# Performance work log

Measured on AMD Instinct MI355X. Metric: run time of the kernel, lower is better.

Reference implementation:

```python
import jax, jax.numpy as jnp
import numpy as np

N_HEADS = 16


def setup_inputs() -> dict:
    key = jax.random.key(0)
    ks = jax.random.split(key, 4)
    B, S, E = 4, 2048, 1024
    x = jax.random.normal(ks[0], (B, S, E), dtype=jnp.float32)
    w_attn = jax.random.normal(ks[1], (E, 3 * E), dtype=jnp.float32) * 0.02
    b_attn = jnp.zeros((3 * E,), dtype=jnp.float32)
    w_proj = jax.random.normal(ks[2], (E, E), dtype=jnp.float32) * 0.02
    b_proj = jnp.zeros((E,), dtype=jnp.float32)
    return {"x": x, "w_attn": w_attn, "b_attn": b_attn, "w_proj": w_proj, "b_proj": b_proj}


def reference(x, w_attn, b_attn, w_proj, b_proj):
    B, S, E = x.shape
    H = N_HEADS
    D = E // H
    # fused QKV projection (Conv1D: x @ W + b)
    qkv = x @ w_attn + b_attn                     # [B, S, 3E]
    q, k, v = jnp.split(qkv, 3, axis=-1)          # each [B, S, E]
    q = q.reshape(B, S, H, D).transpose(0, 2, 1, 3)  # [B, H, S, D]
    k = k.reshape(B, S, H, D).transpose(0, 2, 1, 3)
    v = v.reshape(B, S, H, D).transpose(0, 2, 1, 3)
    # scaled QK^T
    scores = jnp.einsum('bhqd,bhkd->bhqk', q, k) / jnp.sqrt(jnp.asarray(D, dtype=x.dtype))
    # causal mask via where with dtype-min fill (matches torch.where(c_m, w, finfo.min))
    causal = jnp.tril(jnp.ones((S, S), dtype=bool))  # [S, S]
    scores = jnp.where(causal[None, None, :, :], scores, jnp.finfo(scores.dtype).min)
    attn = jax.nn.softmax(scores, axis=-1)        # [B, H, S, S]
    o = jnp.einsum('bhqk,bhkd->bhqd', attn, v)    # [B, H, S, D]
    o = o.transpose(0, 2, 1, 3).reshape(B, S, E)  # merge heads
    return o @ w_proj + b_proj                    # output projection
```

## Files before the change

kernel.cpp:

```cpp
#include <hip/hip_runtime.h>
#include <stdint.h>


typedef __bf16 bf16;
typedef __bf16 bf16x4 __attribute__((ext_vector_type(4)));
typedef __bf16 bf16x8 __attribute__((ext_vector_type(8)));
typedef float  f32x4  __attribute__((ext_vector_type(4)));

#define DEV __device__ __forceinline__

DEV void async_copy16(bf16* lds, const bf16* g) {
  __builtin_amdgcn_global_load_lds(
      (__attribute__((address_space(1))) void*)(uintptr_t)g,
      (__attribute__((address_space(3))) void*)(uint32_t)(uintptr_t)lds,
      16, 0, 0);
}

__global__ __launch_bounds__(256) void cast_x_kernel(const float* __restrict__ in,
                                                     bf16* __restrict__ out, int n4) {
  int i = blockIdx.x * blockDim.x + threadIdx.x;
  int stride = gridDim.x * blockDim.x;
  for (; i < n4; i += stride) {
    float4 v = ((const float4*)in)[i];
    bf16x4 o = { (bf16)v.x, (bf16)v.y, (bf16)v.z, (bf16)v.w };
    *(bf16x4*)(out + (size_t)i * 4) = o;
  }
}

__global__ __launch_bounds__(256) void transpose_cast_kernel(const float* __restrict__ W,
                                                             bf16* __restrict__ Wt,
                                                             int Kd, int Nd) {
  __shared__ alignas(16) bf16 T[64 * 80];
  const int t = threadIdx.x;
  const int n0 = blockIdx.x * 64;
  const int k0 = blockIdx.y * 64;
#pragma unroll
  for (int i = 0; i < 4; ++i) {
    int idx = t + i * 256;
    int r  = idx >> 4;
    int c4 = (idx & 15) * 4;
    float4 v = *(const float4*)(W + (size_t)(k0 + r) * Nd + n0 + c4);
    bf16x4 o = { (bf16)v.x, (bf16)v.y, (bf16)v.z, (bf16)v.w };
    *(bf16x4*)(&T[r * 80 + c4]) = o;
  }
  __syncthreads();
#pragma unroll
  for (int i = 0; i < 2; ++i) {
    int idx = t + i * 256;
    int n = idx >> 3;
    int c = idx & 7;
    bf16x8 o;
#pragma unroll
    for (int j = 0; j < 8; ++j) o[j] = T[(c * 8 + j) * 80 + n];
    *(bf16x8*)(Wt + (size_t)(n0 + n) * Kd + k0 + c * 8) = o;
  }
}

template <typename OutT, bool FUSE_VT>
__global__ __launch_bounds__(512, 4) void gemm256_kernel(const bf16* __restrict__ A,
                                                         const bf16* __restrict__ Bt,
                                                         const float* __restrict__ bias,
                                                         OutT* __restrict__ C,
                                                         bf16* __restrict__ vtout,
                                                         int M, int N, int K,
                                                         float qscale, int qcols,
                                                         int nbx) {
  __shared__ alignas(16) bf16 As[3][256 * 32];
  __shared__ alignas(16) bf16 Bs[3][128 * 32];

  const int tid  = threadIdx.x;
  const int lane = tid & 63;
  const int w    = tid >> 6;
  const int wm = w >> 1, wn = w & 1;
  const int l15 = lane & 15, l16 = lane >> 4;

  const int nwg = (int)gridDim.x;
  const int cpx = nwg >> 3;
  const int swz = ((int)blockIdx.x & 7) * cpx + ((int)blockIdx.x >> 3);
  const int m0 = (swz / nbx) * 256;
  const int n0 = (swz % nbx) * 128;

  const int c0  = w * 64 + lane;
  const int rA0 = c0 >> 2, sA0 = c0 & 3;
  const int rA1 = rA0 + 128;
  const bf16* srcA0 = A  + (size_t)(m0 + rA0) * K + 8 * (sA0 ^ ((rA0 >> 1) & 3));
  const bf16* srcA1 = A  + (size_t)(m0 + rA1) * K + 8 * (sA0 ^ ((rA1 >> 1) & 3));
  const bf16* srcB  = Bt + (size_t)(n0 + rA0) * K + 8 * (sA0 ^ ((rA0 >> 1) & 3));

#define STAGE_TILE(buf, kt)                                       \
  {                                                               \
    const int k0_ = (kt) * 32;                                    \
    async_copy16(&As[buf][(w * 64) * 8],         srcA0 + k0_);    \
    async_copy16(&As[buf][(512 + w * 64) * 8],   srcA1 + k0_);    \
    async_copy16(&Bs[buf][(w * 64) * 8],         srcB  + k0_);    \
  }

  f32x4 acc[4][4];
  f32x4 zf = {0.f, 0.f, 0.f, 0.f};
#pragma unroll
  for (int i = 0; i < 4; ++i)
#pragma unroll
    for (int j = 0; j < 4; ++j) acc[i][j] = zf;

  const int KT = K >> 5;
  STAGE_TILE(0, 0)
  STAGE_TILE(1, 1)

  const int soff = 8 * (l16 ^ ((l15 >> 1) & 3));

  int bufc = 0;
  int bufs = 2;
  for (int kt = 0; kt < KT; ++kt) {
    if (kt < KT - 1) { asm volatile("s_waitcnt vmcnt(3)" ::: "memory"); }
    else             { asm volatile("s_waitcnt vmcnt(0)" ::: "memory"); }
    __builtin_amdgcn_s_barrier();
    asm volatile("" ::: "memory");
    if (kt + 2 < KT) STAGE_TILE(bufs, kt + 2)

    bf16x8 bfr[4], afr[4];
#pragma unroll
    for (int n = 0; n < 4; ++n) {
      int rb = wn * 64 + n * 16 + l15;
      bfr[n] = *(const bf16x8*)(&Bs[bufc][rb * 32 + soff]);
    }
#pragma unroll
    for (int m = 0; m < 4; ++m) {
      int ra = wm * 64 + m * 16 + l15;
      afr[m] = *(const bf16x8*)(&As[bufc][ra * 32 + soff]);
    }
    __builtin_amdgcn_s_setprio(1);
#pragma unroll
    for (int m = 0; m < 4; ++m)
#pragma unroll
      for (int n = 0; n < 4; ++n)
        acc[m][n] = __builtin_amdgcn_mfma_f32_16x16x32_bf16(afr[m], bfr[n], acc[m][n], 0, 0, 0);
    __builtin_amdgcn_s_setprio(0);
    asm volatile("" ::: "memory");
    bufc = (bufc == 2) ? 0 : bufc + 1;
    bufs = (bufs == 2) ? 0 : bufs + 1;
  }

#pragma unroll
  for (int n = 0; n < 4; ++n) {
    int col = n0 + wn * 64 + n * 16 + l15;
    float bb = bias[col];
    if (FUSE_VT && col >= 2048) {
      int hh = (col - 2048) >> 6, d = (col - 2048) & 63;
#pragma unroll
      for (int m = 0; m < 4; ++m) {
#pragma unroll
        for (int reg = 0; reg < 4; ++reg) {
          int row = m0 + wm * 64 + m * 16 + l16 * 4 + reg;
          int s = row & 2047;
          int key = s & 63;
          int pos = (key & 32) | (((key >> 2) & 3) << 3) | (((key >> 4) & 1) << 2) | (key & 3);
          size_t vtaddr = ((size_t)((row >> 11) * 16 + hh) * 64 + d) * 2048 + (s & ~63) + pos;
          vtout[vtaddr] = (bf16)(acc[m][n][reg] + bb);
        }
      }
    } else {
      float sc2 = (col < qcols) ? qscale : 1.0f;
#pragma unroll
      for (int m = 0; m < 4; ++m) {
#pragma unroll
        for (int reg = 0; reg < 4; ++reg) {
          int row = m0 + wm * 64 + m * 16 + l16 * 4 + reg;
          C[(size_t)row * N + col] = (OutT)((acc[m][n][reg] + bb) * sc2);
        }
      }
    }
  }
#undef STAGE_TILE
}

__global__ __launch_bounds__(256, 4) void flash_kernel(const bf16* __restrict__ qkv,
                                                       const bf16* __restrict__ vt,
                                                       bf16* __restrict__ obuf) {
  constexpr int S = 2048, E3 = 3072;
  __shared__ alignas(16) bf16 Ks[2][64 * 64];
  __shared__ alignas(16) bf16 Vs[2][64 * 64];

  const int tid  = threadIdx.x;
  const int lane = tid & 63;
  const int w    = tid >> 6;
  const int t  = 15 - (int)blockIdx.x;
  const int bh = blockIdx.y;
  const int b = bh >> 4, h = bh & 15;
  const int l15 = lane & 15, l16 = lane >> 4;

  const int sr  = lane >> 3;
  const int scc = lane & 7;
  const int r0 = w * 16 + sr;
  const int r1 = w * 16 + 8 + sr;
  const bf16* kst0 = qkv + (size_t)(b * S + r0) * E3 + 1024 + h * 64 + 8 * (scc ^ sr);
  const bf16* kst1 = qkv + (size_t)(b * S + r1) * E3 + 1024 + h * 64 + 8 * (scc ^ sr);
  const bf16* vst0 = vt + (size_t)(bh * 64 + r0) * S + 8 * (scc ^ sr);
  const bf16* vst1 = vt + (size_t)(bh * 64 + r1) * S + 8 * (scc ^ sr);

  const int xsw = l15 & 7;
  const uint32_t rdA = (uint32_t)(l15 * 128 + 16 * (l16 ^ xsw));
  const uint32_t rdB = (uint32_t)(l15 * 128 + 16 * ((4 + l16) ^ xsw));

#define KV_STAGE(buf, kv0_)                                          \
  {                                                                  \
    async_copy16(Ks[buf] + (w * 2) * 512,     kst0 + (size_t)(kv0_) * E3); \
    async_copy16(Ks[buf] + (w * 2 + 1) * 512, kst1 + (size_t)(kv0_) * E3); \
    async_copy16(Vs[buf] + (w * 2) * 512,     vst0 + (kv0_));        \
    async_copy16(Vs[buf] + (w * 2 + 1) * 512, vst1 + (kv0_));        \
  }

  const int q0 = t * 128;
  const int wq0 = q0 + w * 32;
  const int nsteps = 2 * t + 2;

  KV_STAGE(0, 0)

  bf16x8 qf[2][2];
  {
    const bf16* qbase = qkv + (size_t)(b * S + wq0) * E3 + h * 64;
#pragma unroll
    for (int s = 0; s < 2; ++s)
#pragma unroll
      for (int dk = 0; dk < 2; ++dk)
        qf[s][dk] = *(const bf16x8*)(qbase + (size_t)(s * 16 + l15) * E3 + (dk * 4 + l16) * 8);
  }

  float lstate[2] = {0.f, 0.f};
  f32x4 oacc[2][4];
  f32x4 zf = {0.f, 0.f, 0.f, 0.f};
#pragma unroll
  for (int s = 0; s < 2; ++s)
#pragma unroll
    for (int i = 0; i < 4; ++i) oacc[s][i] = zf;

  __syncthreads();

#define FLASH_STEP(CUR, STEPIDX)                                                  \
    {                                                                             \
      const int kv0 = (STEPIDX) * 64;                                             \
      if ((STEPIDX) + 1 < nsteps) KV_STAGE((CUR) ^ 1, kv0 + 64)                   \
      if (kv0 <= wq0 + 31) {                     \
        f32x4 sv[2][4];                                                           \
        _Pragma("unroll")                                                         \
        for (int kf = 0; kf < 4; ++kf) { sv[0][kf] = zf; sv[1][kf] = zf; }        \
        __builtin_amdgcn_s_setprio(1);                                            \
        _Pragma("unroll")                                                         \
        for (int kf = 0; kf < 4; ++kf) {                                          \
          bf16x8 k0 = *(const bf16x8*)((const char*)Ks[CUR] + rdA + kf * 2048);   \
          sv[0][kf] = __builtin_amdgcn_mfma_f32_16x16x32_bf16(k0, qf[0][0], sv[0][kf], 0, 0, 0); \
          sv[1][kf] = __builtin_amdgcn_mfma_f32_16x16x32_bf16(k0, qf[1][0], sv[1][kf], 0, 0, 0); \
          bf16x8 k1 = *(const bf16x8*)((const char*)Ks[CUR] + rdB + kf * 2048);   \
          sv[0][kf] = __builtin_amdgcn_mfma_f32_16x16x32_bf16(k1, qf[0][1], sv[0][kf], 0, 0, 0); \
          sv[1][kf] = __builtin_amdgcn_mfma_f32_16x16x32_bf16(k1, qf[1][1], sv[1][kf], 0, 0, 0); \
        }                                                                         \
        __builtin_amdgcn_s_setprio(0);                                            \
        bf16x8 pb[2][2];                                                          \
        _Pragma("unroll")                                                         \
        for (int s = 0; s < 2; ++s) {                                             \
          if (kv0 + 63 > wq0 + s * 16) {                \
            const int qrow_ = wq0 + s * 16 + l15;                                 \
            _Pragma("unroll")                                                     \
            for (int kf = 0; kf < 4; ++kf)                                        \
              _Pragma("unroll")                                                   \
              for (int reg = 0; reg < 4; ++reg) {                                 \
                int key = kv0 + kf * 16 + l16 * 4 + reg;                          \
                if (key > qrow_) sv[s][kf][reg] = -1e30f;                         \
              }                                                                   \
          }                                                                       \
          float rsum = 0.f;                                                       \
          _Pragma("unroll")                                                       \
          for (int kf = 0; kf < 4; ++kf)                                          \
            _Pragma("unroll")                                                     \
            for (int reg = 0; reg < 4; ++reg) {                                   \
              float p = __builtin_amdgcn_exp2f(sv[s][kf][reg]);                   \
              sv[s][kf][reg] = p;                                                 \
              rsum += p;                                                          \
            }                                                                     \
          rsum += __shfl_xor(rsum, 16);                                           \
          rsum += __shfl_xor(rsum, 32);                                           \
          lstate[s] += rsum;                                                      \
          _Pragma("unroll")                                                       \
          for (int kc = 0; kc < 2; ++kc) {                                        \
            bf16x8 tq;                                                            \
            tq[0] = (bf16)sv[s][2 * kc][0];  tq[1] = (bf16)sv[s][2 * kc][1];      \
            tq[2] = (bf16)sv[s][2 * kc][2];  tq[3] = (bf16)sv[s][2 * kc][3];      \
            tq[4] = (bf16)sv[s][2 * kc + 1][0]; tq[5] = (bf16)sv[s][2 * kc + 1][1]; \
            tq[6] = (bf16)sv[s][2 * kc + 1][2]; tq[7] = (bf16)sv[s][2 * kc + 1][3]; \
            pb[s][kc] = tq;                                                       \
          }                                                                       \
        }                                                                         \
        __builtin_amdgcn_s_setprio(1);                                            \
        _Pragma("unroll")                                                         \
        for (int nf = 0; nf < 4; ++nf) {                                          \
          bf16x8 vf0 = *(const bf16x8*)((const char*)Vs[CUR] + rdA + nf * 2048);  \
          oacc[0][nf] = __builtin_amdgcn_mfma_f32_16x16x32_bf16(vf0, pb[0][0], oacc[0][nf], 0, 0, 0); \
          oacc[1][nf] = __builtin_amdgcn_mfma_f32_16x16x32_bf16(vf0, pb[1][0], oacc[1][nf], 0, 0, 0); \
          bf16x8 vf1 = *(const bf16x8*)((const char*)Vs[CUR] + rdB + nf * 2048);  \
          oacc[0][nf] = __builtin_amdgcn_mfma_f32_16x16x32_bf16(vf1, pb[0][1], oacc[0][nf], 0, 0, 0); \
          oacc[1][nf] = __builtin_amdgcn_mfma_f32_16x16x32_bf16(vf1, pb[1][1], oacc[1][nf], 0, 0, 0); \
        }                                                                         \
        __builtin_amdgcn_s_setprio(0);                                            \
      }                                                                           \
      __syncthreads();          \
    }

  for (int step = 0; step < nsteps; step += 2) {
    FLASH_STEP(0, step)
    FLASH_STEP(1, step + 1)
  }
#undef FLASH_STEP

#pragma unroll
  for (int s = 0; s < 2; ++s) {
    float inv = 1.0f / lstate[s];
    int qrow = wq0 + s * 16 + l15;
#pragma unroll
    for (int nf = 0; nf < 4; ++nf) {
      bf16x4 o4 = { (bf16)(oacc[s][nf][0] * inv), (bf16)(oacc[s][nf][1] * inv),
                    (bf16)(oacc[s][nf][2] * inv), (bf16)(oacc[s][nf][3] * inv) };
      *(bf16x4*)(obuf + (size_t)(b * S + qrow) * 1024 + h * 64 + nf * 16 + l16 * 4) = o4;
    }
  }
#undef KV_STAGE
}

extern "C" void kernel_launch(void* const* d_in, const int* in_sizes, int n_in,
                              void* d_out, int out_size, void* d_ws, size_t ws_size,
                              hipStream_t stream) {
  (void)in_sizes; (void)n_in; (void)out_size; (void)ws_size;
  const float* x      = (const float*)d_in[0];
  const float* w_attn = (const float*)d_in[1];
  const float* b_attn = (const float*)d_in[2];
  const float* w_proj = (const float*)d_in[3];
  const float* b_proj = (const float*)d_in[4];
  float* out = (float*)d_out;

  char* ws = (char*)d_ws;
  bf16* xb  = (bf16*)(ws + 0);
  bf16* wat = (bf16*)(ws + 16777216);
  bf16* wpt = (bf16*)(ws + 23068672);
  bf16* qkv = (bf16*)(ws + 25165824);
  bf16* vt  = (bf16*)(ws + 75497472);
  bf16* ob  = (bf16*)(ws + 92274688);

  const float QSCALE = 0.18033688011112042f;

  cast_x_kernel<<<2048, 256, 0, stream>>>(x, xb, 8192 * 1024 / 4);
  transpose_cast_kernel<<<dim3(48, 16), 256, 0, stream>>>(w_attn, wat, 1024, 3072);
  transpose_cast_kernel<<<dim3(16, 16), 256, 0, stream>>>(w_proj, wpt, 1024, 1024);
  gemm256_kernel<bf16, true><<<768, 512, 0, stream>>>(xb, wat, b_attn, qkv, vt,
                                                      8192, 3072, 1024, QSCALE, 1024, 24);
  flash_kernel<<<dim3(16, 64), 256, 0, stream>>>(qkv, vt, ob);
  gemm256_kernel<float, false><<<256, 512, 0, stream>>>(ob, wpt, b_proj, out, nullptr,
                                                        8192, 1024, 1024, 1.0f, 0, 8);
}
```

Before: 173.0 us.

## Pair causal query tiles per block and triple-buffer KV with one barrier per step

Each flash block now handles two query tiles (t and 15-t), so every block does the same amount of causal work and the grid is halved. KV staging moves from double to triple buffering with a prefetch distance of two tiles. Explicit vmcnt waits plus a single barrier per step replace the trailing __syncthreads. This targets causal load imbalance and exposed load latency, at the cost of more LDS per block (possibly lower occupancy) and fewer blocks, which leaves less parallelism.

```diff
diff --git a/kernel.cpp b/kernel.cpp
--- a/kernel.cpp
+++ b/kernel.cpp
@@ -177,13 +177,13 @@
                                                        const bf16* __restrict__ vt,
                                                        bf16* __restrict__ obuf) {
   constexpr int S = 2048, E3 = 3072;
-  __shared__ alignas(16) bf16 Ks[2][64 * 64];
-  __shared__ alignas(16) bf16 Vs[2][64 * 64];
+  __shared__ alignas(16) bf16 Ks[3][64 * 64];
+  __shared__ alignas(16) bf16 Vs[3][64 * 64];
 
   const int tid  = threadIdx.x;
   const int lane = tid & 63;
   const int w    = tid >> 6;
-  const int t  = 15 - (int)blockIdx.x;
+  const int bx = blockIdx.x;
   const int bh = blockIdx.y;
   const int b = bh >> 4, h = bh & 15;
   const int l15 = lane & 15, l16 = lane >> 4;
@@ -209,116 +209,129 @@
     async_copy16(Vs[buf] + (w * 2 + 1) * 512, vst1 + (kv0_));        \
   }
 
-  const int q0 = t * 128;
-  const int wq0 = q0 + w * 32;
-  const int nsteps = 2 * t + 2;
-
-  KV_STAGE(0, 0)
-
-  bf16x8 qf[2][2];
-  {
-    const bf16* qbase = qkv + (size_t)(b * S + wq0) * E3 + h * 64;
+  for (int half = 0; half < 2; ++half) {
+    const int t = half ? (15 - bx) : bx;
+    const int q0 = t * 128;
+    const int wq0 = q0 + w * 32;
+    const int nsteps = 2 * t + 2;
+
+    KV_STAGE(0, 0)
+    KV_STAGE(1, 64)
+
+    bf16x8 qf[2][2];
+    {
+      const bf16* qbase = qkv + (size_t)(b * S + wq0) * E3 + h * 64;
+#pragma unroll
+      for (int s = 0; s < 2; ++s)
+#pragma unroll
+        for (int dk = 0; dk < 2; ++dk)
+          qf[s][dk] = *(const bf16x8*)(qbase + (size_t)(s * 16 + l15) * E3 + (dk * 4 + l16) * 8);
+    }
+
+    float lstate[2] = {0.f, 0.f};
+    f32x4 oacc[2][4];
+    f32x4 zf = {0.f, 0.f, 0.f, 0.f};
 #pragma unroll
     for (int s = 0; s < 2; ++s)
 #pragma unroll
-      for (int dk = 0; dk < 2; ++dk)
-        qf[s][dk] = *(const bf16x8*)(qbase + (size_t)(s * 16 + l15) * E3 + (dk * 4 + l16) * 8);
-  }
-
-  float lstate[2] = {0.f, 0.f};
-  f32x4 oacc[2][4];
-  f32x4 zf = {0.f, 0.f, 0.f, 0.f};
-#pragma unroll
-  for (int s = 0; s < 2; ++s)
-#pragma unroll
-    for (int i = 0; i < 4; ++i) oacc[s][i] = zf;
-
-  __syncthreads();
-
-#define FLASH_STEP(CUR, STEPIDX)                                                  \
-    {                                                                             \
-      const int kv0 = (STEPIDX) * 64;                                             \
-      if ((STEPIDX) + 1 < nsteps) KV_STAGE((CUR) ^ 1, kv0 + 64)                   \
-      if (kv0 <= wq0 + 31) {                     \
-        f32x4 sv[2][4];                                                           \
-        _Pragma("unroll")                                                         \
-        for (int kf = 0; kf < 4; ++kf) { sv[0][kf] = zf; sv[1][kf] = zf; }        \
-        __builtin_amdgcn_s_setprio(1);                                            \
-        _Pragma("unroll")                                                         \
-        for (int kf = 0; kf < 4; ++kf) {                                          \
-          bf16x8 k0 = *(const bf16x8*)((const char*)Ks[CUR] + rdA + kf * 2048);   \
-          sv[0][kf] = __builtin_amdgcn_mfma_f32_16x16x32_bf16(k0, qf[0][0], sv[0][kf], 0, 0, 0); \
-          sv[1][kf] = __builtin_amdgcn_mfma_f32_16x16x32_bf16(k0, qf[1][0], sv[1][kf], 0, 0, 0); \
-          bf16x8 k1 = *(const bf16x8*)((const char*)Ks[CUR] + rdB + kf * 2048);   \
-          sv[0][kf] = __builtin_amdgcn_mfma_f32_16x16x32_bf16(k1, qf[0][1], sv[0][kf], 0, 0, 0); \
-          sv[1][kf] = __builtin_amdgcn_mfma_f32_16x16x32_bf16(k1, qf[1][1], sv[1][kf], 0, 0, 0); \
-        }                                                                         \
-        __builtin_amdgcn_s_setprio(0);                                            \
-        bf16x8 pb[2][2];                                                          \
-        _Pragma("unroll")                                                         \
-        for (int s = 0; s < 2; ++s) {                                             \
-          if (kv0 + 63 > wq0 + s * 16) {                \
-            const int qrow_ = wq0 + s * 16 + l15;                                 \
-            _Pragma("unroll")                                                     \
-            for (int kf = 0; kf < 4; ++kf)                                        \
-              _Pragma("unroll")                                                   \
-              for (int reg = 0; reg < 4; ++reg) {                                 \
-                int key = kv0 + kf * 16 + l16 * 4 + reg;                          \
-                if (key > qrow_) sv[s][kf][reg] = -1e30f;                         \
-              }                                                                   \
-          }                                                                       \
-          float rsum = 0.f;                                                       \
-          _Pragma("unroll")                                                       \
-          for (int kf = 0; kf < 4; ++kf)                                          \
-            _Pragma("unroll")                                                     \
-            for (int reg = 0; reg < 4; ++reg) {                                   \
-              float p = __builtin_amdgcn_exp2f(sv[s][kf][reg]);                   \
-              sv[s][kf][reg] = p;                                                 \
-              rsum += p;                                                          \
-            }                                                                     \
-          rsum += __shfl_xor(rsum, 16);                                           \
-          rsum += __shfl_xor(rsum, 32);                                           \
-          lstate[s] += rsum;                                                      \
-          _Pragma("unroll")                                                       \
-          for (int kc = 0; kc < 2; ++kc) {                                        \
-            bf16x8 tq;                                                            \
-            tq[0] = (bf16)sv[s][2 * kc][0];  tq[1] = (bf16)sv[s][2 * kc][1];      \
-            tq[2] = (bf16)sv[s][2 * kc][2];  tq[3] = (bf16)sv[s][2 * kc][3];      \
-            tq[4] = (bf16)sv[s][2 * kc + 1][0]; tq[5] = (bf16)sv[s][2 * kc + 1][1]; \
-            tq[6] = (bf16)sv[s][2 * kc + 1][2]; tq[7] = (bf16)sv[s][2 * kc + 1][3]; \
-            pb[s][kc] = tq;                                                       \
-          }                                                                       \
-        }                                                                         \
-        __builtin_amdgcn_s_setprio(1);                                            \
-        _Pragma("unroll")                                                         \
-        for (int nf = 0; nf < 4; ++nf) {                                          \
-          bf16x8 vf0 = *(const bf16x8*)((const char*)Vs[CUR] + rdA + nf * 2048);  \
-          oacc[0][nf] = __builtin_amdgcn_mfma_f32_16x16x32_bf16(vf0, pb[0][0], oacc[0][nf], 0, 0, 0); \
-          oacc[1][nf] = __builtin_amdgcn_mfma_f32_16x16x32_bf16(vf0, pb[1][0], oacc[1][nf], 0, 0, 0); \
-          bf16x8 vf1 = *(const bf16x8*)((const char*)Vs[CUR] + rdB + nf * 2048);  \
-          oacc[0][nf] = __builtin_amdgcn_mfma_f32_16x16x32_bf16(vf1, pb[0][1], oacc[0][nf], 0, 0, 0); \
-          oacc[1][nf] = __builtin_amdgcn_mfma_f32_16x16x32_bf16(vf1, pb[1][1], oacc[1][nf], 0, 0, 0); \
-        }                                                                         \
-        __builtin_amdgcn_s_setprio(0);                                            \
-      }                                                                           \
-      __syncthreads();          \
-    }
-
-  for (int step = 0; step < nsteps; step += 2) {
-    FLASH_STEP(0, step)
-    FLASH_STEP(1, step + 1)
-  }
-#undef FLASH_STEP
-
-#pragma unroll
-  for (int s = 0; s < 2; ++s) {
-    float inv = 1.0f / lstate[s];
-    int qrow = wq0 + s * 16 + l15;
-#pragma unroll
-    for (int nf = 0; nf < 4; ++nf) {
-      bf16x4 o4 = { (bf16)(oacc[s][nf][0] * inv), (bf16)(oacc[s][nf][1] * inv),
-                    (bf16)(oacc[s][nf][2] * inv), (bf16)(oacc[s][nf][3] * inv) };
-      *(bf16x4*)(obuf + (size_t)(b * S + qrow) * 1024 + h * 64 + nf * 16 + l16 * 4) = o4;
+      for (int i = 0; i < 4; ++i) oacc[s][i] = zf;
+
+    __syncthreads();
+
+    int bufc = 0;
+    int bufs = 2;
+    for (int kt = 0; kt < nsteps; ++kt) {
+      if (kt > 0) {
+        if (kt < nsteps - 1) { asm volatile("s_waitcnt vmcnt(4)" ::: "memory"); }
+        else                 { asm volatile("s_waitcnt vmcnt(0)" ::: "memory"); }
+        __builtin_amdgcn_s_barrier();
+        asm volatile("" ::: "memory");
+      }
+      if (kt + 2 < nsteps) KV_STAGE(bufs, (kt + 2) * 64)
+
+      const int kv0 = kt * 64;
+      if (kv0 <= wq0 + 31) {
+        const char* Kb = (const char*)Ks[bufc];
+        const char* Vb = (const char*)Vs[bufc];
+        f32x4 sv[2][4];
+#pragma unroll
+        for (int kf = 0; kf < 4; ++kf) { sv[0][kf] = zf; sv[1][kf] = zf; }
+        __builtin_amdgcn_s_setprio(1);
+#pragma unroll
+        for (int kf = 0; kf < 4; ++kf) {
+          bf16x8 k0 = *(const bf16x8*)(Kb + rdA + kf * 2048);
+          sv[0][kf] = __builtin_amdgcn_mfma_f32_16x16x32_bf16(k0, qf[0][0], sv[0][kf], 0, 0, 0);
+          sv[1][kf] = __builtin_amdgcn_mfma_f32_16x16x32_bf16(k0, qf[1][0], sv[1][kf], 0, 0, 0);
+          bf16x8 k1 = *(const bf16x8*)(Kb + rdB + kf * 2048);
+          sv[0][kf] = __builtin_amdgcn_mfma_f32_16x16x32_bf16(k1, qf[0][1], sv[0][kf], 0, 0, 0);
+          sv[1][kf] = __builtin_amdgcn_mfma_f32_16x16x32_bf16(k1, qf[1][1], sv[1][kf], 0, 0, 0);
+        }
+        __builtin_amdgcn_s_setprio(0);
+
+        bf16x8 pb[2][2];
+#pragma unroll
+        for (int s = 0; s < 2; ++s) {
+          if (kv0 + 63 > wq0 + s * 16) {
+            const int qrow_ = wq0 + s * 16 + l15;
+#pragma unroll
+            for (int kf = 0; kf < 4; ++kf)
+#pragma unroll
+              for (int reg = 0; reg < 4; ++reg) {
+                int key = kv0 + kf * 16 + l16 * 4 + reg;
+                if (key > qrow_) sv[s][kf][reg] = -1e30f;
+              }
+          }
+          float rsum = 0.f;
+#pragma unroll
+          for (int kf = 0; kf < 4; ++kf)
+#pragma unroll
+            for (int reg = 0; reg < 4; ++reg) {
+              float p = __builtin_amdgcn_exp2f(sv[s][kf][reg]);
+              sv[s][kf][reg] = p;
+              rsum += p;
+            }
+          rsum += __shfl_xor(rsum, 16);
+          rsum += __shfl_xor(rsum, 32);
+          lstate[s] += rsum;
+#pragma unroll
+          for (int kc = 0; kc < 2; ++kc) {
+            bf16x8 tq;
+            tq[0] = (bf16)sv[s][2 * kc][0];  tq[1] = (bf16)sv[s][2 * kc][1];
+            tq[2] = (bf16)sv[s][2 * kc][2];  tq[3] = (bf16)sv[s][2 * kc][3];
+            tq[4] = (bf16)sv[s][2 * kc + 1][0]; tq[5] = (bf16)sv[s][2 * kc + 1][1];
+            tq[6] = (bf16)sv[s][2 * kc + 1][2]; tq[7] = (bf16)sv[s][2 * kc + 1][3];
+            pb[s][kc] = tq;
+          }
+        }
+
+        __builtin_amdgcn_s_setprio(1);
+#pragma unroll
+        for (int nf = 0; nf < 4; ++nf) {
+          bf16x8 vf0 = *(const bf16x8*)(Vb + rdA + nf * 2048);
+          oacc[0][nf] = __builtin_amdgcn_mfma_f32_16x16x32_bf16(vf0, pb[0][0], oacc[0][nf], 0, 0, 0);
+          oacc[1][nf] = __builtin_amdgcn_mfma_f32_16x16x32_bf16(vf0, pb[1][0], oacc[1][nf], 0, 0, 0);
+          bf16x8 vf1 = *(const bf16x8*)(Vb + rdB + nf * 2048);
+          oacc[0][nf] = __builtin_amdgcn_mfma_f32_16x16x32_bf16(vf1, pb[0][1], oacc[0][nf], 0, 0, 0);
+          oacc[1][nf] = __builtin_amdgcn_mfma_f32_16x16x32_bf16(vf1, pb[1][1], oacc[1][nf], 0, 0, 0);
+        }
+        __builtin_amdgcn_s_setprio(0);
+      }
+      bufc = (bufc == 2) ? 0 : bufc + 1;
+      bufs = (bufs == 2) ? 0 : bufs + 1;
+    }
+
+    __syncthreads();
+
+#pragma unroll
+    for (int s = 0; s < 2; ++s) {
+      float inv = 1.0f / lstate[s];
+      int qrow = wq0 + s * 16 + l15;
+#pragma unroll
+      for (int nf = 0; nf < 4; ++nf) {
+        bf16x4 o4 = { (bf16)(oacc[s][nf][0] * inv), (bf16)(oacc[s][nf][1] * inv),
+                      (bf16)(oacc[s][nf][2] * inv), (bf16)(oacc[s][nf][3] * inv) };
+        *(bf16x4*)(obuf + (size_t)(b * S + qrow) * 1024 + h * 64 + nf * 16 + l16 * 4) = o4;
+      }
     }
   }
 #undef KV_STAGE
@@ -350,7 +363,7 @@
   transpose_cast_kernel<<<dim3(16, 16), 256, 0, stream>>>(w_proj, wpt, 1024, 1024);
   gemm256_kernel<bf16, true><<<768, 512, 0, stream>>>(xb, wat, b_attn, qkv, vt,
                                                       8192, 3072, 1024, QSCALE, 1024, 24);
-  flash_kernel<<<dim3(16, 64), 256, 0, stream>>>(qkv, vt, ob);
+  flash_kernel<<<dim3(8, 64), 256, 0, stream>>>(qkv, vt, ob);
   gemm256_kernel<float, false><<<256, 512, 0, stream>>>(ob, wpt, b_proj, out, nullptr,
                                                         8192, 1024, 1024, 1.0f, 0, 8);
 }
```

Result: faster. 159.2 us (-8.0%).
